# Performance work log

Hardware: AMD Instinct MI355X
Metric: run time of the kernel (lower is better)

## Reference

```python
import jax, jax.numpy as jnp
import numpy as np

N_NODES = 50000
N_EDGES = 600000
IN_DIM = 128
OUT_DIM = 128
N_REL = 10
LN_EPS = 1e-5


def setup_inputs() -> dict:
    key = jax.random.key(0)
    ks = jax.random.split(key, 6)
    x = jax.random.normal(ks[0], (N_NODES, IN_DIM), dtype=jnp.float32)
    edge_index = jax.random.randint(ks[1], (2, N_EDGES), 0, N_NODES, dtype=jnp.int64)
    edge_type = jax.random.randint(ks[2], (N_EDGES,), 0, N_REL, dtype=jnp.int64)
    # Xavier-uniform relation weights, zero relation bias (matches _reset_parameters)
    limit = float(np.sqrt(6.0 / (IN_DIM + OUT_DIM)))
    relation_weights = jax.random.uniform(ks[3], (N_REL, IN_DIM, OUT_DIM), minval=-limit, maxval=limit, dtype=jnp.float32)
    relation_bias = jnp.zeros((N_REL, OUT_DIM), dtype=jnp.float32)
    # nn.Linear default init: kaiming-uniform-ish; use uniform(-1/sqrt(in), 1/sqrt(in))
    bound = float(1.0 / np.sqrt(IN_DIM))
    w_self = jax.random.uniform(ks[4], (OUT_DIM, IN_DIM), minval=-bound, maxval=bound, dtype=jnp.float32)
    b_self = jax.random.uniform(ks[5], (OUT_DIM,), minval=-bound, maxval=bound, dtype=jnp.float32)
    ln_gamma = jnp.ones((OUT_DIM,), dtype=jnp.float32)
    ln_beta = jnp.zeros((OUT_DIM,), dtype=jnp.float32)
    return {
        "x": x,
        "edge_index": edge_index,
        "edge_type": edge_type,
        "relation_weights": relation_weights,
        "relation_bias": relation_bias,
        "w_self": w_self,
        "b_self": b_self,
        "ln_gamma": ln_gamma,
        "ln_beta": ln_beta,
    }


def reference(x, edge_index, edge_type, relation_weights, relation_bias, w_self, b_self, ln_gamma, ln_beta):
    num_nodes = x.shape[0]
    # self-loop linear
    out = x @ w_self.T + b_self  # [N, out]
    # transform all nodes under every relation once: [R, N, out]
    xr = jnp.einsum('nd,rdo->rno', x, relation_weights)
    src, dst = edge_index[0], edge_index[1]
    # gather per-edge messages for its relation, add relation bias
    messages = xr[edge_type, src] + relation_bias[edge_type]  # [E, out]
    # scatter-add messages to destination nodes
    out = out + jax.ops.segment_sum(messages, dst, num_segments=num_nodes)
    # LayerNorm over last dim
    mean = jnp.mean(out, axis=-1, keepdims=True)
    var = jnp.mean(jnp.square(out - mean), axis=-1, keepdims=True)
    return (out - mean) * jax.lax.rsqrt(var + LN_EPS) * ln_gamma + ln_beta
```

## Files before the change

### kernel.cpp

```cpp
#include <hip/hip_runtime.h>
#include <stdint.h>

#define N_NODES 50000
#define N_EDGES 600000
#define DIM 128
#define LN_EPS 1e-5f
#define NB_SCAN 49
#define NB_HIST 2344
#define NB_PW 704
#define NB_XR_ROW 391
#define NB_XR (NB_XR_ROW * 11)

typedef __attribute__((ext_vector_type(8)))  short bf16x8;
typedef __attribute__((ext_vector_type(16))) float f32x16;

__device__ __forceinline__ float bf2f(unsigned short u) {
    union { uint32_t i; float f; } v;
    v.i = ((uint32_t)u) << 16;
    return v.f;
}
__device__ __forceinline__ unsigned short f2bf(float f) {
    union { float f; uint32_t i; } v;
    v.f = f;
    uint32_t lsb = (v.i >> 16) & 1u;
    uint32_t r = v.i + 0x7FFFu + lsb;
    return (unsigned short)(r >> 16);
}
__device__ __forceinline__ uint32_t pack2bf(float a, float b) {
    return (uint32_t)f2bf(a) | ((uint32_t)f2bf(b) << 16);
}
__device__ __forceinline__ float loadf(const void* p, size_t i, int isbf) {
    if (isbf) return bf2f(((const unsigned short*)p)[i]);
    return ((const float*)p)[i];
}
__device__ __forceinline__ int detect_bf(const void* gamma) {
    return (((const uint32_t*)gamma)[0] == 0x3F803F80u) ? 1 : 0;
}

__global__ __launch_bounds__(256) void build_pre(
    const int* __restrict__ ei, int* __restrict__ deg,
    const void* __restrict__ rw, const void* __restrict__ wself,
    const void* __restrict__ gamma, unsigned short* __restrict__ Wt)
{
    int b = blockIdx.x;
    if (b < NB_HIST) {
        int e = b * 256 + threadIdx.x;
        if (e < N_EDGES) atomicAdd(&deg[ei[N_EDGES + e]], 1);
    } else {
        int i = (b - NB_HIST) * 256 + threadIdx.x;
        int isbf = detect_bf(gamma);
        int g = i >> 14;
        int r = i & 16383;
        int o = r >> 7;
        int k = r & 127;
        float val = (g < 10) ? loadf(rw, (size_t)g * 16384 + (size_t)k * 128 + o, isbf)
                             : loadf(wself, (size_t)o * 128 + k, isbf);
        Wt[i] = f2bf(val);
    }
}

__global__ __launch_bounds__(1024) void scan1(
    const int* __restrict__ deg, int* __restrict__ pfx, int* __restrict__ btot)
{
    __shared__ int sm[1024];
    int t = threadIdx.x;
    int n = blockIdx.x * 1024 + t;
    int d = (n < N_NODES) ? deg[n] : 0;
    sm[t] = d;
    __syncthreads();
    for (int off = 1; off < 1024; off <<= 1) {
        int v = (t >= off) ? sm[t - off] : 0;
        __syncthreads();
        sm[t] += v;
        __syncthreads();
    }
    if (n < N_NODES) pfx[n] = sm[t] - d;
    if (t == 1023) btot[blockIdx.x] = sm[1023];
}

__global__ __launch_bounds__(256) void rowstart(
    const int* __restrict__ pfx, const int* __restrict__ btot,
    int* __restrict__ rs, int* __restrict__ cursor)
{
    __shared__ int sm[256];
    int b = blockIdx.x, t = threadIdx.x;
    int q = b >> 2;
    sm[t] = (t < q) ? btot[t] : 0;
    __syncthreads();
    for (int off = 128; off > 0; off >>= 1) {
        if (t < off) sm[t] += sm[t + off];
        __syncthreads();
    }
    int S = sm[0];
    int i = b * 256 + t;
    if (i < N_NODES) {
        int v = pfx[i] + S;
        rs[i] = v;
        cursor[i] = v;
    }
    if (b == 0 && t == 0) rs[N_NODES] = N_EDGES;
}

__global__ __launch_bounds__(256) void scatter(
    const int* __restrict__ ei, const int* __restrict__ et,
    int* __restrict__ cursor, uint32_t* __restrict__ eidx)
{
    int e = blockIdx.x * 256 + threadIdx.x;
    if (e < N_EDGES) {
        int d = ei[N_EDGES + e];
        int pos = atomicAdd(&cursor[d], 1);
        eidx[pos] = ((uint32_t)et[e] << 20) | (uint32_t)ei[e];
    }
}

__global__ __launch_bounds__(256, 4) void xr_kernel(
    const void* __restrict__ x, const unsigned short* __restrict__ Wt,
    const void* __restrict__ gamma, unsigned short* __restrict__ xr)
{
    __shared__ __align__(16) unsigned short Ws[128][136];

    const int tid = threadIdx.x;
    const int w = tid >> 6;
    const int lane = tid & 63;
    const int half = lane >> 5;
    const int l31 = lane & 31;
    const int bx = blockIdx.x;
    const int rb = bx / 11;
    const int g = bx - rb * 11;
    const int m_base = rb * 128;
    const int isbf = detect_bf(gamma);

    {
        const unsigned short* Wg = Wt + (size_t)g * DIM * DIM;
#pragma unroll
        for (int j = 0; j < 8; ++j) {
            int c = tid + 256 * j;
            *(uint4*)&Ws[c >> 4][(c & 15) * 8] = *(const uint4*)(Wg + (size_t)c * 8);
        }
    }

    const int myrow = min(m_base + w * 32 + l31, N_NODES - 1);
    bf16x8 af[8];
    if (isbf) {
        const unsigned short* xp = (const unsigned short*)x + (size_t)myrow * DIM + half * 8;
#pragma unroll
        for (int ks = 0; ks < 8; ++ks)
            af[ks] = *(const bf16x8*)(xp + ks * 16);
    } else {
        const float* xp = (const float*)x + (size_t)myrow * DIM + half * 8;
#pragma unroll
        for (int ks = 0; ks < 8; ++ks) {
            float4 f0 = *(const float4*)(xp + ks * 16);
            float4 f1 = *(const float4*)(xp + ks * 16 + 4);
            bf16x8 a;
            a[0] = (short)f2bf(f0.x); a[1] = (short)f2bf(f0.y);
            a[2] = (short)f2bf(f0.z); a[3] = (short)f2bf(f0.w);
            a[4] = (short)f2bf(f1.x); a[5] = (short)f2bf(f1.y);
            a[6] = (short)f2bf(f1.z); a[7] = (short)f2bf(f1.w);
            af[ks] = a;
        }
    }
    __syncthreads();

    f32x16 acc[4];
#pragma unroll
    for (int nt = 0; nt < 4; ++nt)
#pragma unroll
        for (int r = 0; r < 16; ++r) acc[nt][r] = 0.f;

#pragma unroll
    for (int ks = 0; ks < 8; ++ks) {
        int ko = ks * 16 + half * 8;
#pragma unroll
        for (int nt = 0; nt < 4; ++nt) {
            bf16x8 b = *(const bf16x8*)&Ws[nt * 32 + l31][ko];
            acc[nt] = __builtin_amdgcn_mfma_f32_32x32x16_bf16(af[ks], b, acc[nt], 0, 0, 0);
        }
    }

    uint32_t* xo32 = (uint32_t*)xr;
#pragma unroll
    for (int r = 0; r < 16; r += 2) {
        const int row0 = (r & 3) + 8 * (r >> 2) + 4 * half;
        const int nodeE = m_base + w * 32 + row0;
        const int node = nodeE + (l31 & 1);
        uint32_t pk[4];
#pragma unroll
        for (int nt = 0; nt < 4; ++nt) {
            float v0 = acc[nt][r], v1 = acc[nt][r + 1];
            float o0 = __shfl_xor(v0, 1, 64);
            float o1 = __shfl_xor(v1, 1, 64);
            pk[nt] = (l31 & 1) ? pack2bf(o1, v1) : pack2bf(v0, o0);
        }
        if (node < N_NODES) {
            uint32_t* op = xo32 + ((size_t)g * N_NODES + node) * 64 + (l31 >> 1);
#pragma unroll
            for (int nt = 0; nt < 4; ++nt)
                op[nt * 16] = pk[nt];
        }
    }
}

__global__ __launch_bounds__(256) void node_kernel(
    const unsigned short* __restrict__ xr, const uint32_t* __restrict__ eidx,
    const int* __restrict__ rs,
    const void* __restrict__ rb, const void* __restrict__ bself,
    const void* __restrict__ gamma, const void* __restrict__ beta,
    void* __restrict__ out)
{
    __shared__ float rbA[10][64], rbB[10][64];
    __shared__ float bsA[64], bsB[64];

    const int tid = threadIdx.x;
    const int w = tid >> 6;
    const int lane = tid & 63;
    const int isbf = detect_bf(gamma);

    for (int i = tid; i < 640; i += 256) {
        int r = i >> 6, c = i & 63;
        rbA[r][c] = loadf(rb, (size_t)r * DIM + 2 * c, isbf);
        rbB[r][c] = loadf(rb, (size_t)r * DIM + 2 * c + 1, isbf);
    }
    if (tid < 64) {
        bsA[tid] = loadf(bself, 2 * tid, isbf);
        bsB[tid] = loadf(bself, 2 * tid + 1, isbf);
    }
    __syncthreads();

    const int n = blockIdx.x * 4 + w;
    const uint32_t* xr32 = (const uint32_t*)xr;

    float a0, a1;
    {
        uint32_t u = xr32[((size_t)10 * N_NODES + n) * 64 + lane];
        a0 = bsA[lane] + bf2f((unsigned short)u);
        a1 = bsB[lane] + bf2f((unsigned short)(u >> 16));
    }

    const int s0 = rs[n], s1 = rs[n + 1];
    for (int base = s0; base < s1; base += 64) {
        int nb = min(64, s1 - base);
        uint32_t ev = (lane < nb) ? eidx[base + lane] : 0u;
        int i = 0;
        for (; i + 4 <= nb; i += 4) {
            uint32_t q0 = __builtin_amdgcn_readlane(ev, i);
            uint32_t q1 = __builtin_amdgcn_readlane(ev, i + 1);
            uint32_t q2 = __builtin_amdgcn_readlane(ev, i + 2);
            uint32_t q3 = __builtin_amdgcn_readlane(ev, i + 3);
            int r0 = (int)(q0 >> 20), r1 = (int)(q1 >> 20);
            int r2 = (int)(q2 >> 20), r3 = (int)(q3 >> 20);
            uint32_t u0 = xr32[((size_t)r0 * N_NODES + (q0 & 0xFFFFFu)) * 64 + lane];
            uint32_t u1 = xr32[((size_t)r1 * N_NODES + (q1 & 0xFFFFFu)) * 64 + lane];
            uint32_t u2 = xr32[((size_t)r2 * N_NODES + (q2 & 0xFFFFFu)) * 64 + lane];
            uint32_t u3 = xr32[((size_t)r3 * N_NODES + (q3 & 0xFFFFFu)) * 64 + lane];
            a0 += bf2f((unsigned short)u0) + rbA[r0][lane];
            a1 += bf2f((unsigned short)(u0 >> 16)) + rbB[r0][lane];
            a0 += bf2f((unsigned short)u1) + rbA[r1][lane];
            a1 += bf2f((unsigned short)(u1 >> 16)) + rbB[r1][lane];
            a0 += bf2f((unsigned short)u2) + rbA[r2][lane];
            a1 += bf2f((unsigned short)(u2 >> 16)) + rbB[r2][lane];
            a0 += bf2f((unsigned short)u3) + rbA[r3][lane];
            a1 += bf2f((unsigned short)(u3 >> 16)) + rbB[r3][lane];
        }
        for (; i < nb; ++i) {
            uint32_t q = __builtin_amdgcn_readlane(ev, i);
            int r = (int)(q >> 20);
            uint32_t u = xr32[((size_t)r * N_NODES + (q & 0xFFFFFu)) * 64 + lane];
            a0 += bf2f((unsigned short)u) + rbA[r][lane];
            a1 += bf2f((unsigned short)(u >> 16)) + rbB[r][lane];
        }
    }

    float s = a0 + a1, s2 = a0 * a0 + a1 * a1;
#pragma unroll
    for (int msk = 1; msk <= 32; msk <<= 1) {
        s  += __shfl_xor(s,  msk, 64);
        s2 += __shfl_xor(s2, msk, 64);
    }
    float mean = s * (1.f / DIM);
    float var = s2 * (1.f / DIM) - mean * mean;
    float inv = rsqrtf(var + LN_EPS);
    float g0 = loadf(gamma, 2 * lane, isbf),     b0 = loadf(beta, 2 * lane, isbf);
    float g1 = loadf(gamma, 2 * lane + 1, isbf), b1 = loadf(beta, 2 * lane + 1, isbf);
    float y0 = (a0 - mean) * inv * g0 + b0;
    float y1 = (a1 - mean) * inv * g1 + b1;
    if (isbf) {
        ((uint32_t*)out)[(size_t)n * 64 + lane] = pack2bf(y0, y1);
    } else {
        ((float2*)out)[(size_t)n * 64 + lane] = make_float2(y0, y1);
    }
}

extern "C" void kernel_launch(void* const* d_in, const int* in_sizes, int n_in,
                              void* d_out, int out_size, void* d_ws, size_t ws_size,
                              hipStream_t stream) {
    const void* x     = d_in[0];
    const int*  ei    = (const int*)d_in[1];
    const int*  et    = (const int*)d_in[2];
    const void* rw    = d_in[3];
    const void* rb    = d_in[4];
    const void* wself = d_in[5];
    const void* bself = d_in[6];
    const void* gamma = d_in[7];
    const void* beta  = d_in[8];

    char* ws = (char*)d_ws;
    unsigned short* Wt     = (unsigned short*)(ws + 256);
    int*            deg    = (int*)(ws + 360704);
    int*            pfx    = (int*)(ws + 560704);
    int*            btot   = (int*)(ws + 760704);
    int*            rs     = (int*)(ws + 760960);
    int*            cursor = (int*)(ws + 961024);
    uint32_t*       eidx   = (uint32_t*)(ws + 1161024);
    unsigned short* xr     = (unsigned short*)(ws + 3561088);

    hipMemsetAsync(deg, 0, N_NODES * sizeof(int), stream);
    build_pre<<<NB_HIST + NB_PW, 256, 0, stream>>>(ei, deg, rw, wself, gamma, Wt);
    scan1<<<NB_SCAN, 1024, 0, stream>>>(deg, pfx, btot);
    rowstart<<<(N_NODES + 255) / 256, 256, 0, stream>>>(pfx, btot, rs, cursor);
    scatter<<<(N_EDGES + 255) / 256, 256, 0, stream>>>(ei, et, cursor, eidx);
    xr_kernel<<<NB_XR, 256, 0, stream>>>(x, Wt, gamma, xr);
    node_kernel<<<N_NODES / 4, 256, 0, stream>>>(xr, eidx, rs, rb, bself, gamma, beta, d_out);
}
```

Baseline: 261.2 us.

## Loop over relations inside xr block, split output columns into quarters

The relation-transform GEMM grid changes from one block per (row tile, relation) to one block per (row tile, 32-column quarter). Each block keeps its x fragment in registers and loops over all 11 weight matrices, loading only a 32x128 weight slice per iteration into a smaller shared buffer. This cuts redundant x reads and shared-memory footprint but adds per-iteration barriers and serialized weight loads, and the launch-bounds occupancy hint is removed.

```diff
diff --git a/kernel.cpp b/kernel.cpp
--- a/kernel.cpp
+++ b/kernel.cpp
@@ -8,8 +8,7 @@
 #define NB_SCAN 49
 #define NB_HIST 2344
 #define NB_PW 704
-#define NB_XR_ROW 391
-#define NB_XR (NB_XR_ROW * 11)
+#define NB_XR (391 * 4)
 
 typedef __attribute__((ext_vector_type(8)))  short bf16x8;
 typedef __attribute__((ext_vector_type(16))) float f32x16;
@@ -113,11 +112,11 @@
     }
 }
 
-__global__ __launch_bounds__(256, 4) void xr_kernel(
+__global__ __launch_bounds__(256) void xr_kernel(
     const void* __restrict__ x, const unsigned short* __restrict__ Wt,
     const void* __restrict__ gamma, unsigned short* __restrict__ xr)
 {
-    __shared__ __align__(16) unsigned short Ws[128][136];
+    __shared__ __align__(16) unsigned short Ws[32][136];
 
     const int tid = threadIdx.x;
     const int w = tid >> 6;
@@ -125,19 +124,10 @@
     const int half = lane >> 5;
     const int l31 = lane & 31;
     const int bx = blockIdx.x;
-    const int rb = bx / 11;
-    const int g = bx - rb * 11;
+    const int rb = bx >> 2;
+    const int cq = bx & 3;
     const int m_base = rb * 128;
     const int isbf = detect_bf(gamma);
-
-    {
-        const unsigned short* Wg = Wt + (size_t)g * DIM * DIM;
-#pragma unroll
-        for (int j = 0; j < 8; ++j) {
-            int c = tid + 256 * j;
-            *(uint4*)&Ws[c >> 4][(c & 15) * 8] = *(const uint4*)(Wg + (size_t)c * 8);
-        }
-    }
 
     const int myrow = min(m_base + w * 32 + l31, N_NODES - 1);
     bf16x8 af[8];
@@ -160,43 +150,43 @@
             af[ks] = a;
         }
     }
-    __syncthreads();
-
-    f32x16 acc[4];
-#pragma unroll
-    for (int nt = 0; nt < 4; ++nt)
-#pragma unroll
-        for (int r = 0; r < 16; ++r) acc[nt][r] = 0.f;
-
-#pragma unroll
-    for (int ks = 0; ks < 8; ++ks) {
-        int ko = ks * 16 + half * 8;
-#pragma unroll
-        for (int nt = 0; nt < 4; ++nt) {
-            bf16x8 b = *(const bf16x8*)&Ws[nt * 32 + l31][ko];
-            acc[nt] = __builtin_amdgcn_mfma_f32_32x32x16_bf16(af[ks], b, acc[nt], 0, 0, 0);
-        }
-    }
 
     uint32_t* xo32 = (uint32_t*)xr;
-#pragma unroll
-    for (int r = 0; r < 16; r += 2) {
-        const int row0 = (r & 3) + 8 * (r >> 2) + 4 * half;
-        const int nodeE = m_base + w * 32 + row0;
-        const int node = nodeE + (l31 & 1);
-        uint32_t pk[4];
-#pragma unroll
-        for (int nt = 0; nt < 4; ++nt) {
-            float v0 = acc[nt][r], v1 = acc[nt][r + 1];
+
+    for (int g = 0; g < 11; ++g) {
+        __syncthreads();
+        {
+            const unsigned short* Wg = Wt + (size_t)g * DIM * DIM + (size_t)cq * 32 * DIM;
+#pragma unroll
+            for (int j = 0; j < 2; ++j) {
+                int c = tid + 256 * j;
+                *(uint4*)&Ws[c >> 4][(c & 15) * 8] = *(const uint4*)(Wg + (size_t)c * 8);
+            }
+        }
+        __syncthreads();
+
+        f32x16 acc;
+#pragma unroll
+        for (int r = 0; r < 16; ++r) acc[r] = 0.f;
+
+#pragma unroll
+        for (int ks = 0; ks < 8; ++ks) {
+            int ko = ks * 16 + half * 8;
+            bf16x8 b = *(const bf16x8*)&Ws[l31][ko];
+            acc = __builtin_amdgcn_mfma_f32_32x32x16_bf16(af[ks], b, acc, 0, 0, 0);
+        }
+
+#pragma unroll
+        for (int rr = 0; rr < 16; rr += 2) {
+            const int row0 = (rr & 3) + 8 * (rr >> 2) + 4 * half;
+            const int nodeE = m_base + w * 32 + row0;
+            const int node = nodeE + (l31 & 1);
+            float v0 = acc[rr], v1 = acc[rr + 1];
             float o0 = __shfl_xor(v0, 1, 64);
             float o1 = __shfl_xor(v1, 1, 64);
-            pk[nt] = (l31 & 1) ? pack2bf(o1, v1) : pack2bf(v0, o0);
-        }
-        if (node < N_NODES) {
-            uint32_t* op = xo32 + ((size_t)g * N_NODES + node) * 64 + (l31 >> 1);
-#pragma unroll
-            for (int nt = 0; nt < 4; ++nt)
-                op[nt * 16] = pk[nt];
+            uint32_t pk = (l31 & 1) ? pack2bf(o1, v1) : pack2bf(v0, o0);
+            if (node < N_NODES)
+                xo32[((size_t)g * N_NODES + node) * 64 + cq * 16 + (l31 >> 1)] = pk;
         }
     }
 }
```

Measured after the change: 255.6 us. 1.02x faster.
